# Kernel tuning notes

Hardware: AMD Instinct MI355X
Metric: run time of the kernel (lower is better)

## Reference

```python
import jax, jax.numpy as jnp
import numpy as np

N = 500000
D = 256
B = 1024  # number of graphs / segments


def setup_inputs() -> dict:
    key = jax.random.key(0)
    k1, k2, k3, k4 = jax.random.split(key, 4)
    x = jax.random.normal(k1, (N, D), dtype=jnp.float32)
    batch = jnp.sort(jax.random.randint(k2, (N,), 0, B))
    W1 = jax.random.normal(k3, (D, D // 2), dtype=jnp.float32) * (1.0 / np.sqrt(D))
    b1 = jnp.zeros((D // 2,), dtype=jnp.float32)
    W2 = jax.random.normal(k4, (D // 2, 1), dtype=jnp.float32) * (1.0 / np.sqrt(D // 2))
    b2 = jnp.zeros((1,), dtype=jnp.float32)
    return {"x": x, "batch": batch, "W1": W1, "b1": b1, "W2": W2, "b2": b2}


def _segment_mean(vals, seg, num_segments):
    # torch_scatter scatter_mean: sum / count (0 for empty segments)
    s = jax.ops.segment_sum(vals, seg, num_segments=num_segments)
    cnt = jax.ops.segment_sum(jnp.ones((vals.shape[0],), vals.dtype), seg,
                              num_segments=num_segments)
    return s / jnp.maximum(cnt, 1.0)[:, None]


def reference(x, batch, W1, b1, W2, b2):
    n = x.shape[0]
    # attention MLP -> (N, 1)
    h = jax.nn.relu(x @ W1 + b1)
    w = h @ W2 + b2
    # global max-shifted exp (as in source: w - w.max())
    w = jnp.exp(w - jnp.max(w))
    # denom = scatter_mean(w, batch)[batch] * N
    mean_w = _segment_mean(w, batch, B)            # (B, 1)
    denom = mean_w[batch] * jnp.float32(n)          # (N, 1)
    # pooled = scatter_mean(w * x / (denom + 1e-8), batch)
    pooled = _segment_mean(w * x / (denom + 1e-8), batch, B)  # (B, D)
    return pooled
```

## Files before the change

### kernel.cpp

```cpp
#include <hip/hip_runtime.h>
#include <math.h>

typedef float f32x4 __attribute__((ext_vector_type(4)));
typedef __attribute__((ext_vector_type(8))) _Float16 f16x8;
typedef __attribute__((ext_vector_type(4))) _Float16 f16x4;

#define DD 256
#define DH 128
#define NSPLIT 2
#define TROWS 64

__global__ void ap_setup(const float* __restrict__ W1, _Float16* __restrict__ w1f,
                         const int* __restrict__ batch, int* __restrict__ start,
                         int nrows, int bseg) {
  const int bid = blockIdx.x;
  if (bid < 16) {
    int t = bid * 256 + threadIdx.x;
    int l = t & 63;
    int tile = t >> 6;
    int kt = tile >> 3, nt = tile & 7;
    int kbase = kt * 32 + (l >> 4) * 8;
    int col = nt * 16 + (l & 15);
#pragma unroll
    for (int j = 0; j < 8; ++j) {
      w1f[t * 8 + j] = (_Float16)W1[(kbase + j) * DH + col];
    }
  } else {
    int i = (bid - 16) * 256 + threadIdx.x;
    if (i >= nrows) return;
    int c = batch[i];
    int p = (i == 0) ? -1 : batch[i - 1];
    for (int b = p + 1; b <= c; ++b) start[b] = i;
    if (i == nrows - 1) {
      for (int b = c + 1; b <= bseg; ++b) start[b] = nrows;
    }
  }
}

__global__ __launch_bounds__(512)
void ap_fused(const float* __restrict__ x, const _Float16* __restrict__ w1f,
              const float* __restrict__ b1, const float* __restrict__ W2,
              const float* __restrict__ b2, const int* __restrict__ start,
              float* __restrict__ pooledPart, float* __restrict__ mPart,
              float* __restrict__ swPart, int nrows) {
  __shared__ __align__(16) _Float16 xsh[2][TROWS * 256];
  __shared__ __align__(16) _Float16 sB[64 * 64 * 8];
  __shared__ float praw[2][2][TROWS];
  __shared__ float swArr[8];

  const int tid = threadIdx.x;
  const int wv = tid >> 6;
  const int g = wv >> 1;
  const int hw = wv & 1;
  const int l = tid & 63;
  const int l15 = l & 15, lhi = l >> 4;

  const int bi = blockIdx.x;
  const int b = bi >> 1;
  const int q = bi & (NSPLIT - 1);
  const int s0 = start[b], e0 = start[b + 1];
  const int cnt = e0 - s0;
  const int L = (cnt + NSPLIT - 1) >> 1;
  const int s = s0 + q * L;
  int pe = s + L;
  if (pe > e0) pe = e0;
  const int e = pe;
  const int ce = (e > 0) ? (e - 1) : 0;

  {
    const f32x4* src = (const f32x4*)w1f;
    f32x4* dst = (f32x4*)sB;
#pragma unroll
    for (int it = 0; it < 8; ++it) dst[it * 512 + tid] = src[it * 512 + tid];
  }

  float b1f[4], w2f[4];
#pragma unroll
  for (int nt = 0; nt < 4; ++nt) {
    const int idx = (hw * 4 + nt) * 16 + l15;
    b1f[nt] = b1[idx];
    w2f[nt] = W2[idx];
  }
  const float bb = *b2;
  const float NI = -__builtin_inff();

  f32x4 accp = {0.f, 0.f, 0.f, 0.f};
  float m = NI;
  float swv = 0.f;

  f32x4 xcol[8], xnext[8];
#pragma unroll
  for (int i = 0; i < 8; ++i) {
    const int R = g * 16 + hw * 8 + i;
    int grow = s + R;
    if (grow > ce) grow = ce;
    if (grow < 0) grow = 0;
    xcol[i] = *(const f32x4*)(x + (size_t)grow * DD + l * 4);
  }
#pragma unroll
  for (int i = 0; i < 8; ++i) {
    const int R = g * 16 + hw * 8 + i;
    const int gp = l ^ ((R & 7) << 1);
    f16x4 h4;
#pragma unroll
    for (int j = 0; j < 4; ++j) h4[j] = (_Float16)xcol[i][j];
    *(f16x4*)(xsh[0] + (size_t)(R * 64 + gp) * 4) = h4;
  }
  __syncthreads();

  int buf = 0;
  for (int t0 = s; t0 < e; t0 += TROWS) {
    const bool hasNext = (t0 + TROWS < e);

    if (hasNext) {
#pragma unroll
      for (int i = 0; i < 8; ++i) {
        const int R = g * 16 + hw * 8 + i;
        int grow = t0 + TROWS + R;
        if (grow > ce) grow = ce;
        xnext[i] = *(const f32x4*)(x + (size_t)grow * DD + l * 4);
      }
    }

    f32x4 acc[4];
#pragma unroll
    for (int nt = 0; nt < 4; ++nt) acc[nt] = f32x4{0.f, 0.f, 0.f, 0.f};
    const int Rr = g * 16 + l15;
    const int sxe = (Rr & 7) << 1;
#pragma unroll
    for (int kt = 0; kt < 8; ++kt) {
      const int gp = (kt * 8 + lhi * 2) ^ sxe;
      const f16x8 ah = *(const f16x8*)(xsh[buf] + (size_t)(Rr * 64 + gp) * 4);
#pragma unroll
      for (int nt = 0; nt < 4; ++nt) {
        const f16x8 Bh =
            *((const f16x8*)sB + (size_t)(kt * 8 + hw * 4 + nt) * 64 + l);
        acc[nt] = __builtin_amdgcn_mfma_f32_16x16x32_f16(ah, Bh, acc[nt], 0, 0, 0);
      }
    }

    float pr[4];
#pragma unroll
    for (int r = 0; r < 4; ++r) pr[r] = 0.f;
#pragma unroll
    for (int nt = 0; nt < 4; ++nt) {
#pragma unroll
      for (int r = 0; r < 4; ++r)
        pr[r] += fmaxf(acc[nt][r] + b1f[nt], 0.f) * w2f[nt];
    }
#pragma unroll
    for (int mm = 1; mm < 16; mm <<= 1) {
#pragma unroll
      for (int r = 0; r < 4; ++r) pr[r] += __shfl_xor(pr[r], mm, 64);
    }
    if (l15 == 0) {
#pragma unroll
      for (int r = 0; r < 4; ++r) praw[buf][hw][g * 16 + lhi * 4 + r] = pr[r];
    }

    if (hasNext) {
#pragma unroll
      for (int i = 0; i < 8; ++i) {
        const int R = g * 16 + hw * 8 + i;
        const int gp = l ^ ((R & 7) << 1);
        f16x4 h4;
#pragma unroll
        for (int j = 0; j < 4; ++j) h4[j] = (_Float16)xnext[i][j];
        *(f16x4*)(xsh[buf ^ 1] + (size_t)(R * 64 + gp) * 4) = h4;
      }
    }

    __syncthreads();

    const float tot =
        (t0 + l < e) ? (praw[buf][0][l] + praw[buf][1][l] + bb) : NI;
    float tv = tot;
#pragma unroll
    for (int mm = 1; mm < 64; mm <<= 1) tv = fmaxf(tv, __shfl_xor(tv, mm, 64));
    const float nm = fmaxf(m, tv);
    const float factor = expf(m - nm);
    m = nm;
    accp *= factor;
    swv *= factor;

#pragma unroll
    for (int i = 0; i < 8; ++i) {
      const int R = g * 16 + hw * 8 + i;
      const float wi = expf(__shfl(tot, R, 64) - m);
      swv += wi;
      accp += wi * xcol[i];
    }
#pragma unroll
    for (int i = 0; i < 8; ++i) xcol[i] = xnext[i];
    buf ^= 1;
  }

  __syncthreads();
  float* pooled = (float*)xsh;
  *(f32x4*)(pooled + (size_t)(wv * 256 + l * 4)) = accp;
  if (l == 0) swArr[wv] = swv;
  __syncthreads();
  if (tid < 64) {
    float sum_w = 0.f;
#pragma unroll
    for (int p = 0; p < 8; ++p) sum_w += swArr[p];
    const f32x4* pw = (const f32x4*)pooled;
    f32x4 v = ((pw[0 * 64 + tid] + pw[1 * 64 + tid]) +
               (pw[2 * 64 + tid] + pw[3 * 64 + tid]));
    f32x4 w = ((pw[4 * 64 + tid] + pw[5 * 64 + tid]) +
               (pw[6 * 64 + tid] + pw[7 * 64 + tid]));
    *(f32x4*)(pooledPart + (size_t)bi * DD + tid * 4) = v + w;
    if (tid == 0) { mPart[bi] = m; swPart[bi] = sum_w; }
  }
}

__global__ __launch_bounds__(64)
void ap_final(const float* __restrict__ pooledPart, const float* __restrict__ mPart,
              const float* __restrict__ swPart, const int* __restrict__ start,
              float* __restrict__ out, int nrows) {
  const int b = blockIdx.x;
  const int tid = threadIdx.x;
  const float NI = -__builtin_inff();
  float mq[NSPLIT];
#pragma unroll
  for (int qv = 0; qv < NSPLIT; ++qv) mq[qv] = mPart[b * NSPLIT + qv];
  float m_f = NI;
#pragma unroll
  for (int qv = 0; qv < NSPLIT; ++qv) m_f = fmaxf(m_f, mq[qv]);
  float fac[NSPLIT];
  float sum_w = 0.f;
#pragma unroll
  for (int qv = 0; qv < NSPLIT; ++qv) {
    fac[qv] = (mq[qv] == NI) ? 0.f : expf(mq[qv] - m_f);
    sum_w += swPart[b * NSPLIT + qv] * fac[qv];
  }
  const int cnt = start[b + 1] - start[b];
  const float cntf = (float)(cnt > 0 ? cnt : 1);
  const float scale = 1.0f / (((sum_w / cntf) * (float)nrows + 1e-8f) * cntf);
  f32x4 r = f32x4{0.f, 0.f, 0.f, 0.f};
#pragma unroll
  for (int qv = 0; qv < NSPLIT; ++qv) {
    r += ((const f32x4*)(pooledPart + (size_t)(b * NSPLIT + qv) * DD))[tid] * fac[qv];
  }
  r *= scale;
  *(f32x4*)(out + (size_t)b * DD + tid * 4) = r;
}

extern "C" void kernel_launch(void* const* d_in, const int* in_sizes, int n_in,
                              void* d_out, int out_size, void* d_ws, size_t ws_size,
                              hipStream_t stream) {
  const float* x     = (const float*)d_in[0];
  const int*   batch = (const int*)d_in[1];
  const float* W1    = (const float*)d_in[2];
  const float* b1    = (const float*)d_in[3];
  const float* W2    = (const float*)d_in[4];
  const float* b2    = (const float*)d_in[5];
  float* out = (float*)d_out;

  const int nrows = in_sizes[1];
  const int bseg = out_size / DD;

  float* pooledPart = (float*)d_ws;
  float* mPart  = pooledPart + (size_t)bseg * NSPLIT * DD;
  float* swPart = mPart + bseg * NSPLIT;
  _Float16* w1f = (_Float16*)(swPart + bseg * NSPLIT);
  int* start = (int*)(w1f + 64 * 64 * 8);

  ap_setup<<<16 + (nrows + 255) / 256, 256, 0, stream>>>(W1, w1f, batch, start,
                                                         nrows, bseg);
  ap_fused<<<bseg * NSPLIT, 512, 0, stream>>>(x, w1f, b1, W2, b2, start,
                                              pooledPart, mPart, swPart, nrows);
  ap_final<<<bseg, 64, 0, stream>>>(pooledPart, mPart, swPart, start, out, nrows);
}
```

Before: 144.8 us.

## Hold W1 fragments in registers and split MFMA work by column group

The fused kernel stops staging W1 in shared memory and instead keeps each wave's slice of W1 (two 16-column tiles across all K) in registers. Waves now split the hidden dimension four ways and the rows two ways, and the partial logits are summed from four shared-memory slots instead of two. This removes the shared-memory reads of B fragments inside the MMA loop and frees 64 KB of LDS. In exchange it adds 16 f16x8 registers per thread, which is why launch bounds now allow one block per SM so the compiler has room to spare.

```diff
diff --git a/kernel.cpp b/kernel.cpp
--- a/kernel.cpp
+++ b/kernel.cpp
@@ -37,21 +37,20 @@
   }
 }
 
-__global__ __launch_bounds__(512)
+__global__ __launch_bounds__(512, 1)
 void ap_fused(const float* __restrict__ x, const _Float16* __restrict__ w1f,
               const float* __restrict__ b1, const float* __restrict__ W2,
               const float* __restrict__ b2, const int* __restrict__ start,
               float* __restrict__ pooledPart, float* __restrict__ mPart,
               float* __restrict__ swPart, int nrows) {
   __shared__ __align__(16) _Float16 xsh[2][TROWS * 256];
-  __shared__ __align__(16) _Float16 sB[64 * 64 * 8];
-  __shared__ float praw[2][2][TROWS];
+  __shared__ float praw[2][4][TROWS];
   __shared__ float swArr[8];
 
   const int tid = threadIdx.x;
   const int wv = tid >> 6;
-  const int g = wv >> 1;
-  const int hw = wv & 1;
+  const int np = wv & 3;
+  const int rgp = wv >> 2;
   const int l = tid & 63;
   const int l15 = l & 15, lhi = l >> 4;
 
@@ -67,19 +66,22 @@
   const int e = pe;
   const int ce = (e > 0) ? (e - 1) : 0;
 
-  {
-    const f32x4* src = (const f32x4*)w1f;
-    f32x4* dst = (f32x4*)sB;
-#pragma unroll
-    for (int it = 0; it < 8; ++it) dst[it * 512 + tid] = src[it * 512 + tid];
-  }
-
-  float b1f[4], w2f[4];
-#pragma unroll
-  for (int nt = 0; nt < 4; ++nt) {
-    const int idx = (hw * 4 + nt) * 16 + l15;
-    b1f[nt] = b1[idx];
-    w2f[nt] = W2[idx];
+  f16x8 Breg[16];
+#pragma unroll
+  for (int kt = 0; kt < 8; ++kt) {
+#pragma unroll
+    for (int nt2 = 0; nt2 < 2; ++nt2) {
+      Breg[kt * 2 + nt2] =
+          *((const f16x8*)w1f + (size_t)(kt * 8 + np * 2 + nt2) * 64 + l);
+    }
+  }
+
+  float b1f[2], w2f[2];
+#pragma unroll
+  for (int nt2 = 0; nt2 < 2; ++nt2) {
+    const int idx = (np * 2 + nt2) * 16 + l15;
+    b1f[nt2] = b1[idx];
+    w2f[nt2] = W2[idx];
   }
   const float bb = *b2;
   const float NI = -__builtin_inff();
@@ -91,15 +93,14 @@
   f32x4 xcol[8], xnext[8];
 #pragma unroll
   for (int i = 0; i < 8; ++i) {
-    const int R = g * 16 + hw * 8 + i;
-    int grow = s + R;
+    int grow = s + wv * 8 + i;
     if (grow > ce) grow = ce;
     if (grow < 0) grow = 0;
     xcol[i] = *(const f32x4*)(x + (size_t)grow * DD + l * 4);
   }
 #pragma unroll
   for (int i = 0; i < 8; ++i) {
-    const int R = g * 16 + hw * 8 + i;
+    const int R = wv * 8 + i;
     const int gp = l ^ ((R & 7) << 1);
     f16x4 h4;
 #pragma unroll
@@ -115,53 +116,60 @@
     if (hasNext) {
 #pragma unroll
       for (int i = 0; i < 8; ++i) {
-        const int R = g * 16 + hw * 8 + i;
-        int grow = t0 + TROWS + R;
+        int grow = t0 + TROWS + wv * 8 + i;
         if (grow > ce) grow = ce;
         xnext[i] = *(const f32x4*)(x + (size_t)grow * DD + l * 4);
       }
     }
 
-    f32x4 acc[4];
-#pragma unroll
-    for (int nt = 0; nt < 4; ++nt) acc[nt] = f32x4{0.f, 0.f, 0.f, 0.f};
-    const int Rr = g * 16 + l15;
-    const int sxe = (Rr & 7) << 1;
+    f32x4 acc[2][2];
+#pragma unroll
+    for (int rg2 = 0; rg2 < 2; ++rg2)
+#pragma unroll
+      for (int nt2 = 0; nt2 < 2; ++nt2) acc[rg2][nt2] = f32x4{0.f, 0.f, 0.f, 0.f};
 #pragma unroll
     for (int kt = 0; kt < 8; ++kt) {
-      const int gp = (kt * 8 + lhi * 2) ^ sxe;
-      const f16x8 ah = *(const f16x8*)(xsh[buf] + (size_t)(Rr * 64 + gp) * 4);
-#pragma unroll
-      for (int nt = 0; nt < 4; ++nt) {
-        const f16x8 Bh =
-            *((const f16x8*)sB + (size_t)(kt * 8 + hw * 4 + nt) * 64 + l);
-        acc[nt] = __builtin_amdgcn_mfma_f32_16x16x32_f16(ah, Bh, acc[nt], 0, 0, 0);
-      }
-    }
-
-    float pr[4];
-#pragma unroll
-    for (int r = 0; r < 4; ++r) pr[r] = 0.f;
-#pragma unroll
-    for (int nt = 0; nt < 4; ++nt) {
-#pragma unroll
-      for (int r = 0; r < 4; ++r)
-        pr[r] += fmaxf(acc[nt][r] + b1f[nt], 0.f) * w2f[nt];
+#pragma unroll
+      for (int rg2 = 0; rg2 < 2; ++rg2) {
+        const int Rr = rgp * 32 + rg2 * 16 + l15;
+        const int gp = (kt * 8 + lhi * 2) ^ ((Rr & 7) << 1);
+        const f16x8 ah = *(const f16x8*)(xsh[buf] + (size_t)(Rr * 64 + gp) * 4);
+        acc[rg2][0] =
+            __builtin_amdgcn_mfma_f32_16x16x32_f16(ah, Breg[kt * 2 + 0], acc[rg2][0], 0, 0, 0);
+        acc[rg2][1] =
+            __builtin_amdgcn_mfma_f32_16x16x32_f16(ah, Breg[kt * 2 + 1], acc[rg2][1], 0, 0, 0);
+      }
+    }
+
+    float pr[2][4];
+#pragma unroll
+    for (int rg2 = 0; rg2 < 2; ++rg2) {
+#pragma unroll
+      for (int r = 0; r < 4; ++r) {
+        float t = fmaxf(acc[rg2][0][r] + b1f[0], 0.f) * w2f[0] +
+                  fmaxf(acc[rg2][1][r] + b1f[1], 0.f) * w2f[1];
+        pr[rg2][r] = t;
+      }
     }
 #pragma unroll
     for (int mm = 1; mm < 16; mm <<= 1) {
 #pragma unroll
-      for (int r = 0; r < 4; ++r) pr[r] += __shfl_xor(pr[r], mm, 64);
+      for (int rg2 = 0; rg2 < 2; ++rg2)
+#pragma unroll
+        for (int r = 0; r < 4; ++r) pr[rg2][r] += __shfl_xor(pr[rg2][r], mm, 64);
     }
     if (l15 == 0) {
 #pragma unroll
-      for (int r = 0; r < 4; ++r) praw[buf][hw][g * 16 + lhi * 4 + r] = pr[r];
+      for (int rg2 = 0; rg2 < 2; ++rg2)
+#pragma unroll
+        for (int r = 0; r < 4; ++r)
+          praw[buf][np][rgp * 32 + rg2 * 16 + lhi * 4 + r] = pr[rg2][r];
     }
 
     if (hasNext) {
 #pragma unroll
       for (int i = 0; i < 8; ++i) {
-        const int R = g * 16 + hw * 8 + i;
+        const int R = wv * 8 + i;
         const int gp = l ^ ((R & 7) << 1);
         f16x4 h4;
 #pragma unroll
@@ -172,8 +180,10 @@
 
     __syncthreads();
 
-    const float tot =
-        (t0 + l < e) ? (praw[buf][0][l] + praw[buf][1][l] + bb) : NI;
+    const float tot = (t0 + l < e)
+                          ? (praw[buf][0][l] + praw[buf][1][l] +
+                             praw[buf][2][l] + praw[buf][3][l] + bb)
+                          : NI;
     float tv = tot;
 #pragma unroll
     for (int mm = 1; mm < 64; mm <<= 1) tv = fmaxf(tv, __shfl_xor(tv, mm, 64));
@@ -185,7 +195,7 @@
 
 #pragma unroll
     for (int i = 0; i < 8; ++i) {
-      const int R = g * 16 + hw * 8 + i;
+      const int R = wv * 8 + i;
       const float wi = expf(__shfl(tot, R, 64) - m);
       swv += wi;
       accp += wi * xcol[i];
```

Measured after the change: 152.9 us. 1.06x slower.

## Process each segment in a single block and fuse final normalization

Applied to the files above, without the earlier changes.

Removes the two-way split of each segment across blocks. One block now processes a whole segment and applies the softmax-denominator scaling directly before writing output, which eliminates the separate combine kernel and the partial-result workspace. This trades fewer, longer-running blocks (less parallelism and tail balance) for one fewer launch and less global traffic, and it amortizes the per-block W1 staging over more rows.

```diff
diff --git a/kernel.cpp b/kernel.cpp
--- a/kernel.cpp
+++ b/kernel.cpp
@@ -7,7 +7,6 @@
 
 #define DD 256
 #define DH 128
-#define NSPLIT 2
 #define TROWS 64
 
 __global__ void ap_setup(const float* __restrict__ W1, _Float16* __restrict__ w1f,
@@ -41,8 +40,7 @@
 void ap_fused(const float* __restrict__ x, const _Float16* __restrict__ w1f,
               const float* __restrict__ b1, const float* __restrict__ W2,
               const float* __restrict__ b2, const int* __restrict__ start,
-              float* __restrict__ pooledPart, float* __restrict__ mPart,
-              float* __restrict__ swPart, int nrows) {
+              float* __restrict__ out, int nrows) {
   __shared__ __align__(16) _Float16 xsh[2][TROWS * 256];
   __shared__ __align__(16) _Float16 sB[64 * 64 * 8];
   __shared__ float praw[2][2][TROWS];
@@ -55,16 +53,8 @@
   const int l = tid & 63;
   const int l15 = l & 15, lhi = l >> 4;
 
-  const int bi = blockIdx.x;
-  const int b = bi >> 1;
-  const int q = bi & (NSPLIT - 1);
-  const int s0 = start[b], e0 = start[b + 1];
-  const int cnt = e0 - s0;
-  const int L = (cnt + NSPLIT - 1) >> 1;
-  const int s = s0 + q * L;
-  int pe = s + L;
-  if (pe > e0) pe = e0;
-  const int e = pe;
+  const int b = blockIdx.x;
+  const int s = start[b], e = start[b + 1];
   const int ce = (e > 0) ? (e - 1) : 0;
 
   {
@@ -209,41 +199,12 @@
                (pw[2 * 64 + tid] + pw[3 * 64 + tid]));
     f32x4 w = ((pw[4 * 64 + tid] + pw[5 * 64 + tid]) +
                (pw[6 * 64 + tid] + pw[7 * 64 + tid]));
-    *(f32x4*)(pooledPart + (size_t)bi * DD + tid * 4) = v + w;
-    if (tid == 0) { mPart[bi] = m; swPart[bi] = sum_w; }
-  }
-}
-
-__global__ __launch_bounds__(64)
-void ap_final(const float* __restrict__ pooledPart, const float* __restrict__ mPart,
-              const float* __restrict__ swPart, const int* __restrict__ start,
-              float* __restrict__ out, int nrows) {
-  const int b = blockIdx.x;
-  const int tid = threadIdx.x;
-  const float NI = -__builtin_inff();
-  float mq[NSPLIT];
-#pragma unroll
-  for (int qv = 0; qv < NSPLIT; ++qv) mq[qv] = mPart[b * NSPLIT + qv];
-  float m_f = NI;
-#pragma unroll
-  for (int qv = 0; qv < NSPLIT; ++qv) m_f = fmaxf(m_f, mq[qv]);
-  float fac[NSPLIT];
-  float sum_w = 0.f;
-#pragma unroll
-  for (int qv = 0; qv < NSPLIT; ++qv) {
-    fac[qv] = (mq[qv] == NI) ? 0.f : expf(mq[qv] - m_f);
-    sum_w += swPart[b * NSPLIT + qv] * fac[qv];
-  }
-  const int cnt = start[b + 1] - start[b];
-  const float cntf = (float)(cnt > 0 ? cnt : 1);
-  const float scale = 1.0f / (((sum_w / cntf) * (float)nrows + 1e-8f) * cntf);
-  f32x4 r = f32x4{0.f, 0.f, 0.f, 0.f};
-#pragma unroll
-  for (int qv = 0; qv < NSPLIT; ++qv) {
-    r += ((const f32x4*)(pooledPart + (size_t)(b * NSPLIT + qv) * DD))[tid] * fac[qv];
-  }
-  r *= scale;
-  *(f32x4*)(out + (size_t)b * DD + tid * 4) = r;
+    const int cnt = e - s;
+    const float cntf = (float)(cnt > 0 ? cnt : 1);
+    const float scale = 1.0f / (((sum_w / cntf) * (float)nrows + 1e-8f) * cntf);
+    f32x4 r = (v + w) * scale;
+    *(f32x4*)(out + (size_t)b * DD + tid * 4) = r;
+  }
 }
 
 extern "C" void kernel_launch(void* const* d_in, const int* in_sizes, int n_in,
@@ -260,15 +221,10 @@
   const int nrows = in_sizes[1];
   const int bseg = out_size / DD;
 
-  float* pooledPart = (float*)d_ws;
-  float* mPart  = pooledPart + (size_t)bseg * NSPLIT * DD;
-  float* swPart = mPart + bseg * NSPLIT;
-  _Float16* w1f = (_Float16*)(swPart + bseg * NSPLIT);
+  _Float16* w1f = (_Float16*)d_ws;
   int* start = (int*)(w1f + 64 * 64 * 8);
 
   ap_setup<<<16 + (nrows + 255) / 256, 256, 0, stream>>>(W1, w1f, batch, start,
                                                          nrows, bseg);
-  ap_fused<<<bseg * NSPLIT, 512, 0, stream>>>(x, w1f, b1, W2, b2, start,
-                                              pooledPart, mPart, swPart, nrows);
-  ap_final<<<bseg, 64, 0, stream>>>(pooledPart, mPart, swPart, start, out, nrows);
+  ap_fused<<<bseg, 512, 0, stream>>>(x, w1f, b1, W2, b2, start, out, nrows);
 }
```

New measurement: 130.2 us. 10.1% less time.
